# Optimization experiments

Measured on AMD Instinct MI355X. Metric: run time of the kernel, lower is better.

The kernel has to match this reference:

```python
import jax, jax.numpy as jnp
import numpy as np

B, S, D, H = 4, 2048, 1024, 16
d = D // H
SCALE = d ** -0.5


def setup_inputs() -> dict:
    key = jax.random.key(0)
    k1, k2, k3 = jax.random.split(key, 3)
    x = jax.random.normal(k1, (B, S, D), dtype=jnp.float32)
    # causal keep-mask (True = keep), shape (B, 1, S, S)
    causal = jnp.tril(jnp.ones((S, S), dtype=bool))
    mask = jnp.broadcast_to(causal[None, None, :, :], (B, 1, S, S))
    # nn.Linear(D, 3D, bias=False): weight (3D, D); out_proj weight (D, D)
    w_qkv = jax.random.normal(k2, (3 * D, D), dtype=jnp.float32) * (D ** -0.5)
    w_out = jax.random.normal(k3, (D, D), dtype=jnp.float32) * (D ** -0.5)
    return {"x": x, "mask": mask, "w_qkv": w_qkv, "w_out": w_out}


def reference(x, mask, w_qkv, w_out):
    # qkv projection: y = x @ W^T, split into q, k, v
    qkv = jnp.einsum('bsd,ed->bse', x, w_qkv)  # (B, S, 3D)
    q, k, v = jnp.split(qkv, 3, axis=-1)
    # (B, S, H, d) -> (B, H, S, d)
    q = q.reshape(B, S, H, d).transpose(0, 2, 1, 3)
    k = k.reshape(B, S, H, d).transpose(0, 2, 1, 3)
    v = v.reshape(B, S, H, d).transpose(0, 2, 1, 3)
    # scores (B, H, S, S)
    attn = jnp.einsum('bhqd,bhkd->bhqk', q, k) * SCALE
    attn = jnp.where(mask, attn, -jnp.inf)
    attn = jax.nn.softmax(attn, axis=-1)
    out = jnp.einsum('bhqk,bhkd->bhqd', attn, v)
    out = out.transpose(0, 2, 1, 3).reshape(B, S, D)
    out = jnp.einsum('bsd,ed->bse', out, w_out)
    return out, (k, v)
```

## Files before the change

kernel.cpp:

```cpp
#include <hip/hip_runtime.h>
#include <hip/hip_bf16.h>

typedef __bf16 bf16_t;
typedef bf16_t bf16x8 __attribute__((ext_vector_type(8)));
typedef bf16_t bf16x4 __attribute__((ext_vector_type(4)));
typedef float  f32x4  __attribute__((ext_vector_type(4)));
typedef float  f32x8  __attribute__((ext_vector_type(8)));
typedef float  f32x16 __attribute__((ext_vector_type(16)));

#define B_  4
#define S_  2048
#define D_  1024
#define H_  16
#define HD  64

#define QSCALE 0.1803368801111204f

#define KV_TILE_ELEMS 4096
#define KV_BH_ELEMS   262144

__device__ __forceinline__ void async_copy16(const void* g, void* l) {
    __builtin_amdgcn_global_load_lds((const __attribute__((address_space(1))) void*)g,
                                     (__attribute__((address_space(3))) void*)l,
                                     16, 0, 0);
}

__device__ __forceinline__ float fast_exp2(float x) {
    float r;
    asm("v_exp_f32 %0, %1" : "=v"(r) : "v"(x));
    return r;
}

template<int N>
__device__ __forceinline__ void wait_vmcnt() {
    if constexpr (N == 12)      asm volatile("s_waitcnt vmcnt(12)" ::: "memory");
    else if constexpr (N == 10) asm volatile("s_waitcnt vmcnt(10)" ::: "memory");
    else if constexpr (N == 8)  asm volatile("s_waitcnt vmcnt(8)"  ::: "memory");
    else if constexpr (N == 6)  asm volatile("s_waitcnt vmcnt(6)"  ::: "memory");
    else if constexpr (N == 5)  asm volatile("s_waitcnt vmcnt(5)"  ::: "memory");
    else if constexpr (N == 4)  asm volatile("s_waitcnt vmcnt(4)"  ::: "memory");
    else if constexpr (N == 3)  asm volatile("s_waitcnt vmcnt(3)"  ::: "memory");
    else                        asm volatile("s_waitcnt vmcnt(0)"  ::: "memory");
}

__global__ __launch_bounds__(256) void cvt_kernel(const float* __restrict__ in,
                                                  bf16_t* __restrict__ out, int n4) {
    int i = blockIdx.x * 256 + threadIdx.x;
    if (i >= n4) return;
    float4 f = ((const float4*)in)[i];
    bf16x4 o = { (bf16_t)f.x, (bf16_t)f.y, (bf16_t)f.z, (bf16_t)f.w };
    ((bf16x4*)out)[i] = o;
}

template<int WNS, int MREP, int NREP>
__device__ __forceinline__ void gemm_core256(const bf16_t* __restrict__ A,
                                             const bf16_t* __restrict__ Bt,
                                             int lda, int ldb, int m0, int n0, int K,
                                             bf16_t* LDS, f32x4 acc[MREP][NREP]) {
    constexpr int BM   = (8 / WNS) * MREP * 16;
    constexpr int BN   = WNS * NREP * 16;
    constexpr int BUFE = (BM + BN) * 32;
    constexpr int AI   = BM / 128;
    constexpr int BI   = BN / 128;
    constexpr int LPS  = AI + BI;

    const int lane = threadIdx.x & 63;
    const int wv   = threadIdx.x >> 6;
    const int wm   = wv / WNS, wn = wv % WNS;
    const int lo   = lane & 15, hi = lane >> 4;
    const int srd  = (lo >> 1) & 3;
    const int r_in = lane >> 2;
    const int csw  = (((lane & 3) ^ ((lane >> 3) & 3))) * 8;

    auto stage = [&](int t, int db) {
        const int k0 = t * 32;
        bf16_t* dstA = LDS + db * BUFE;
        bf16_t* dstB = dstA + BM * 32;
        #pragma unroll
        for (int i = 0; i < AI; ++i) {
            const int base = wv * (BM / 8) + i * 16;
            async_copy16(A + (size_t)(m0 + base + r_in) * lda + k0 + csw, dstA + base * 32);
        }
        #pragma unroll
        for (int i = 0; i < BI; ++i) {
            const int base = wv * (BN / 8) + i * 16;
            async_copy16(Bt + (size_t)(n0 + base + r_in) * ldb + k0 + csw, dstB + base * 32);
        }
    };

    auto compute = [&](int db) {
        const bf16_t* as = LDS + db * BUFE;
        const bf16_t* bs = as + BM * 32;
        const int kos = (hi ^ srd) * 8;
        bf16x8 bF[NREP];
        #pragma unroll
        for (int n = 0; n < NREP; ++n)
            bF[n] = *(const bf16x8*)(bs + (wn * (NREP * 16) + n * 16 + lo) * 32 + kos);
        #pragma unroll
        for (int m = 0; m < MREP; ++m) {
            bf16x8 aF = *(const bf16x8*)(as + (wm * (MREP * 16) + m * 16 + lo) * 32 + kos);
            #pragma unroll
            for (int n = 0; n < NREP; ++n)
                acc[m][n] = __builtin_amdgcn_mfma_f32_16x16x32_bf16(aF, bF[n], acc[m][n], 0, 0, 0);
        }
    };

    const int nt = K / 32;
    stage(0, 0); stage(1, 1); stage(2, 2);

    for (int t = 0; t < nt; ++t) {
        const int db = t % 3;
        if (t + 2 < nt)      wait_vmcnt<2 * LPS>();
        else if (t + 1 < nt) wait_vmcnt<LPS>();
        else                 wait_vmcnt<0>();
        __builtin_amdgcn_s_barrier();
        __builtin_amdgcn_sched_barrier(0);
        compute(db);
        __builtin_amdgcn_sched_barrier(0);
        __builtin_amdgcn_s_barrier();
        __builtin_amdgcn_sched_barrier(0);
        if (t + 3 < nt) stage(t + 3, db);
    }
}

__global__ __launch_bounds__(512) void gemm_qkv_kernel(const bf16_t* __restrict__ A,
                                                       const bf16_t* __restrict__ Bt,
                                                       float* __restrict__ out,
                                                       bf16_t* __restrict__ q_ws,
                                                       bf16_t* __restrict__ kv_frag) {
    __shared__ __align__(16) bf16_t LDS[3 * (256 + 384) * 32];
    const int m0 = (blockIdx.x >> 3) * 256;
    const int n0 = (blockIdx.x & 7) * 384;
    f32x4 acc[8][6];
    #pragma unroll
    for (int m = 0; m < 8; ++m)
        #pragma unroll
        for (int n = 0; n < 6; ++n) acc[m][n] = f32x4{0.f, 0.f, 0.f, 0.f};

    gemm_core256<4, 8, 6>(A, Bt, D_, D_, m0, n0, D_, LDS, acc);

    const int lane = threadIdx.x & 63, wv = threadIdx.x >> 6;
    const int wm = wv >> 2, wn = wv & 3;
    const int lo = lane & 15, hi = lane >> 4;
    #pragma unroll
    for (int m = 0; m < 8; ++m) {
        #pragma unroll
        for (int n = 0; n < 6; ++n) {
            const int gcol = n0 + wn * 96 + n * 16 + lo;
            const int sec  = gcol >> 10;
            const int e    = gcol & 1023;
            const int h    = e >> 6, dv = e & 63;
            #pragma unroll
            for (int j4 = 0; j4 < 4; ++j4) {
                const int grow = m0 + wm * 128 + m * 16 + hi * 4 + j4;
                const float v  = acc[m][n][j4];
                const int b = grow >> 11, s = grow & 2047;
                const size_t idx2 = ((((size_t)b * H_ + h) * S_ + s) << 6) + dv;
                if (sec == 0) {
                    q_ws[idx2] = (bf16_t)(v * QSCALE);
                } else if (sec == 1) {
                    out[8388608u + idx2] = v;
                    const int bh   = b * H_ + h;
                    const int tile = s >> 5, ql = s & 31;
                    const int c    = dv >> 4, hb = (dv >> 3) & 1, jj = dv & 7;
                    kv_frag[(((size_t)bh * 64 + tile) * 8 + c) * 512 + hb * 256 + ql * 8 + jj] = (bf16_t)v;
                } else {
                    out[16777216u + idx2] = v;
                }
            }
        }
    }
}

__global__ __launch_bounds__(256) void build_vfrag_kernel(const float* __restrict__ v_f32,
                                                          bf16_t* __restrict__ kv_frag) {
    __shared__ __align__(16) bf16_t T[64][72];
    const int bh = blockIdx.x;
    const int s0 = blockIdx.y * 64;
    const int t  = threadIdx.x;
    {
        const int sl  = t >> 2;
        const int dv0 = (t & 3) * 16;
        const float* src = v_f32 + ((size_t)bh * S_ + s0 + sl) * HD + dv0;
        float tmp[16];
        #pragma unroll
        for (int i = 0; i < 4; ++i) *(float4*)(tmp + i * 4) = ((const float4*)src)[i];
        #pragma unroll
        for (int i = 0; i < 16; ++i) T[dv0 + i][sl] = (bf16_t)tmp[i];
    }
    __syncthreads();
    {
        const int st = t >> 7;
        const int r  = t & 127;
        const int cc = r >> 5;
        const int l  = r & 31;
        const int khi = cc >> 1, hd = cc & 1;
        const int d   = hd * 32 + l;
        const int tile = (s0 >> 5) + st;
        bf16_t* dst = kv_frag + (((size_t)bh * 64 + tile) * 8 + 4 + cc) * 512 + l * 8;
        const int slb = st * 32 + khi * 16;
        *(bf16x8*)(dst)       = *(const bf16x8*)&T[d][slb];
        *(bf16x8*)(dst + 256) = *(const bf16x8*)&T[d][slb + 8];
    }
}

__global__ __launch_bounds__(256) void attn_kernel(const bf16_t* __restrict__ q_ws,
                                                   const bf16_t* __restrict__ kv_frag,
                                                   bf16_t* __restrict__ attn_ws) {
    __shared__ __align__(16) float MRG[2][2][64][20];
    __shared__ float LSUM[2][64];
    __shared__ __align__(16) bf16_t T[2][32][72];
    const int lane = threadIdx.x & 63;
    const int wv   = threadIdx.x >> 6;
    const int blk   = blockIdx.x;
    const int x     = blk & 7;
    const int r     = blk >> 3;
    const int bh    = x + 8 * (r & 7);
    const int pr    = wv >> 1;
    const int khalf = wv & 1;
    const int p     = (r >> 3) * 2 + pr;

    const int ql = lane & 31;
    const int hb = lane >> 5;
    const size_t kv_base = (size_t)bh * (S_ * HD);
    const int b = bh >> 4, h = bh & 15;

    const bf16_t* kvb = kv_frag + (size_t)bh * KV_BH_ELEMS + (size_t)lane * 8;

    auto load_k = [&](int tile, bf16x8 kf[4]) {
        const bf16_t* tp = kvb + (size_t)tile * KV_TILE_ELEMS;
        #pragma unroll
        for (int c = 0; c < 4; ++c) kf[c] = *(const bf16x8*)(tp + c * 512);
    };
    auto load_v = [&](int tile, bf16x8 vf[4]) {
        const bf16_t* tp = kvb + (size_t)tile * KV_TILE_ELEMS + 2048;
        #pragma unroll
        for (int i = 0; i < 4; ++i) vf[i] = *(const bf16x8*)(tp + i * 512);
    };

    #pragma unroll 1
    for (int pass = 0; pass < 2; ++pass) {
        const int qblock = pass ? (63 - p) : p;
        const int q0 = qblock * 32;
        const int nt  = qblock + 1;
        const int mid = nt >> 1;
        const int tstart = khalf ? mid : 0;
        const int tend   = khalf ? nt  : mid;

        bf16x8 qF[4];
        const bf16_t* qrow = q_ws + kv_base + (size_t)(q0 + ql) * HD + hb * 8;
        #pragma unroll
        for (int c = 0; c < 4; ++c) qF[c] = *(const bf16x8*)(qrow + 16 * c);

        f32x16 accT0 = {}, accT1 = {};
        float lsum = 0.f;

        auto compute_tile = [&](const bf16x8 kf[4], const bf16x8 vf[4], bool diag) {
            f32x16 s = {};
            #pragma unroll
            for (int c = 0; c < 4; ++c)
                s = __builtin_amdgcn_mfma_f32_32x32x16_bf16(kf[c], qF[c], s, 0, 0, 0);
            if (diag) {
                #pragma unroll
                for (int rr = 0; rr < 16; ++rr) {
                    const int kloc = (rr & 3) + 8 * (rr >> 2) + 4 * hb;
                    if (kloc > ql) s[rr] = -1e30f;
                }
            }
            #pragma unroll
            for (int rr = 0; rr < 16; ++rr) s[rr] = fast_exp2(s[rr]);
            f32x8 t8 = __builtin_shufflevector(s, s, 0, 1, 2, 3, 4, 5, 6, 7) +
                       __builtin_shufflevector(s, s, 8, 9, 10, 11, 12, 13, 14, 15);
            f32x4 t4 = __builtin_shufflevector(t8, t8, 0, 1, 2, 3) +
                       __builtin_shufflevector(t8, t8, 4, 5, 6, 7);
            lsum += (t4[0] + t4[1]) + (t4[2] + t4[3]);

            unsigned w[8];
            #pragma unroll
            for (int i = 0; i < 8; ++i) {
                unsigned d;
                asm("v_cvt_pk_bf16_f32 %0, %1, %2" : "=v"(d) : "v"(s[2 * i]), "v"(s[2 * i + 1]));
                w[i] = d;
            }
            union { unsigned u[4]; bf16x8 v; } pf0, pf1;
            {
                auto r0 = __builtin_amdgcn_permlane32_swap(w[0], w[2], false, false);
                auto r1 = __builtin_amdgcn_permlane32_swap(w[1], w[3], false, false);
                pf0.u[0] = r0[0]; pf0.u[1] = r1[0]; pf0.u[2] = r0[1]; pf0.u[3] = r1[1];
            }
            {
                auto r0 = __builtin_amdgcn_permlane32_swap(w[4], w[6], false, false);
                auto r1 = __builtin_amdgcn_permlane32_swap(w[5], w[7], false, false);
                pf1.u[0] = r0[0]; pf1.u[1] = r1[0]; pf1.u[2] = r0[1]; pf1.u[3] = r1[1];
            }

            accT0 = __builtin_amdgcn_mfma_f32_32x32x16_bf16(vf[0], pf0.v, accT0, 0, 0, 0);
            accT1 = __builtin_amdgcn_mfma_f32_32x32x16_bf16(vf[1], pf0.v, accT1, 0, 0, 0);
            accT0 = __builtin_amdgcn_mfma_f32_32x32x16_bf16(vf[2], pf1.v, accT0, 0, 0, 0);
            accT1 = __builtin_amdgcn_mfma_f32_32x32x16_bf16(vf[3], pf1.v, accT1, 0, 0, 0);
        };

        int t = tstart;
        for (; t + 1 < tend; t += 2) {
            bf16x8 kA[4], vA[4], kB[4], vB[4];
            load_k(t, kA);
            load_v(t, vA);
            load_k(t + 1, kB);
            load_v(t + 1, vB);
            compute_tile(kA, vA, t == qblock);
            compute_tile(kB, vB, (t + 1) == qblock);
        }
        if (t < tend) {
            bf16x8 kA[4], vA[4];
            load_k(t, kA);
            load_v(t, vA);
            compute_tile(kA, vA, t == qblock);
        }

        if (khalf) {
            *(f32x16*)&MRG[pr][0][lane][0] = accT0;
            *(f32x16*)&MRG[pr][1][lane][0] = accT1;
            LSUM[pr][lane] = lsum;
        }
        __syncthreads();
        if (!khalf) {
            accT0 += *(const f32x16*)&MRG[pr][0][lane][0];
            accT1 += *(const f32x16*)&MRG[pr][1][lane][0];
            lsum  += LSUM[pr][lane];
            const float ltot = lsum + __shfl_xor(lsum, 32, 64);
            const float inv  = 1.0f / ltot;
            #pragma unroll
            for (int rr = 0; rr < 16; ++rr) {
                const int dl = (rr & 3) + 8 * (rr >> 2) + 4 * hb;
                T[pr][ql][dl]      = (bf16_t)(accT0[rr] * inv);
                T[pr][ql][32 + dl] = (bf16_t)(accT1[rr] * inv);
            }
            asm volatile("s_waitcnt lgkmcnt(0)" ::: "memory");
            #pragma unroll
            for (int it = 0; it < 4; ++it) {
                const int ch  = it * 64 + lane;
                const int row = ch >> 3, c8 = ch & 7;
                bf16x8 o = *(const bf16x8*)&T[pr][row][c8 * 8];
                *(bf16x8*)(attn_ws + ((size_t)(b * S_ + q0 + row)) * D_ + h * HD + c8 * 8) = o;
            }
        }
        __syncthreads();
    }
}

__global__ __launch_bounds__(512) void gemm_out_kernel(const bf16_t* __restrict__ A,
                                                       const bf16_t* __restrict__ Bt,
                                                       float* __restrict__ out) {
    __shared__ __align__(16) bf16_t LDS[3 * (256 + 128) * 32];
    const int m0 = blockIdx.y * 256, n0 = blockIdx.x * 128;
    f32x4 acc[4][4];
    #pragma unroll
    for (int m = 0; m < 4; ++m)
        #pragma unroll
        for (int n = 0; n < 4; ++n) acc[m][n] = f32x4{0.f, 0.f, 0.f, 0.f};

    gemm_core256<2, 4, 4>(A, Bt, D_, D_, m0, n0, D_, LDS, acc);

    const int lane = threadIdx.x & 63, wv = threadIdx.x >> 6;
    const int wm = wv >> 1, wn = wv & 1;
    const int lo = lane & 15, hi = lane >> 4;
    #pragma unroll
    for (int m = 0; m < 4; ++m) {
        #pragma unroll
        for (int n = 0; n < 4; ++n) {
            const int gcol = n0 + wn * 64 + n * 16 + lo;
            #pragma unroll
            for (int j = 0; j < 4; ++j) {
                const int grow = m0 + wm * 64 + m * 16 + hi * 4 + j;
                out[(size_t)grow * D_ + gcol] = acc[m][n][j];
            }
        }
    }
}

extern "C" void kernel_launch(void* const* d_in, const int* in_sizes, int n_in,
                              void* d_out, int out_size, void* d_ws, size_t ws_size,
                              hipStream_t stream) {
    (void)in_sizes; (void)n_in; (void)out_size; (void)ws_size;
    const float* x     = (const float*)d_in[0];
    const float* w_qkv = (const float*)d_in[2];
    const float* w_out = (const float*)d_in[3];
    float* out = (float*)d_out;
    char* ws = (char*)d_ws;

    bf16_t* x_bf    = (bf16_t*)(ws);
    bf16_t* wqkv_bf = (bf16_t*)(ws + 16777216);
    bf16_t* wout_bf = (bf16_t*)(ws + 23068672);
    bf16_t* q_ws    = (bf16_t*)(ws + 25165824);
    bf16_t* kv_frag = (bf16_t*)(ws + 41943040);
    bf16_t* attn_ws = (bf16_t*)(ws + 75497472);

    cvt_kernel<<<8192, 256, 0, stream>>>(x, x_bf, 2097152);
    cvt_kernel<<<3072, 256, 0, stream>>>(w_qkv, wqkv_bf, 786432);
    cvt_kernel<<<1024, 256, 0, stream>>>(w_out, wout_bf, 262144);

    gemm_qkv_kernel<<<256, 512, 0, stream>>>(x_bf, wqkv_bf, out, q_ws, kv_frag);
    build_vfrag_kernel<<<dim3(64, 32), 256, 0, stream>>>(out + 16777216, kv_frag);
    attn_kernel<<<1024, 256, 0, stream>>>(q_ws, kv_frag, attn_ws);
    gemm_out_kernel<<<dim3(8, 32), 512, 0, stream>>>(attn_ws, wout_bf, out);
}
```

Measured before the change: 175.0 us.

## Rewrite QKV GEMM with 256x256 tiles and interleaved 8-wave async-load pipeline

Replaces the generic gemm_core256 call in the QKV projection with a hand-scheduled main loop. It uses 256x256 output tiles (384 blocks instead of 256), a 64-wide K step with double-buffered XOR-swizzled LDS, and async global-to-LDS loads split into halves that are issued between MFMA quarter-steps. The aim is better CU coverage on the 256-CU part and hiding load latency behind MFMA work using setprio and fine-grained barriers. In exchange it adds many more barriers per K step and needs a larger LDS footprint (128KB).

After: 176.5 us. About the same (+0.9%).

```diff
diff --git a/kernel.cpp b/kernel.cpp
--- a/kernel.cpp
+++ b/kernel.cpp
@@ -33,13 +33,11 @@
 
 template<int N>
 __device__ __forceinline__ void wait_vmcnt() {
-    if constexpr (N == 12)      asm volatile("s_waitcnt vmcnt(12)" ::: "memory");
-    else if constexpr (N == 10) asm volatile("s_waitcnt vmcnt(10)" ::: "memory");
+    if constexpr (N == 10)      asm volatile("s_waitcnt vmcnt(10)" ::: "memory");
     else if constexpr (N == 8)  asm volatile("s_waitcnt vmcnt(8)"  ::: "memory");
     else if constexpr (N == 6)  asm volatile("s_waitcnt vmcnt(6)"  ::: "memory");
     else if constexpr (N == 5)  asm volatile("s_waitcnt vmcnt(5)"  ::: "memory");
     else if constexpr (N == 4)  asm volatile("s_waitcnt vmcnt(4)"  ::: "memory");
-    else if constexpr (N == 3)  asm volatile("s_waitcnt vmcnt(3)"  ::: "memory");
     else                        asm volatile("s_waitcnt vmcnt(0)"  ::: "memory");
 }
 
@@ -128,25 +126,138 @@
                                                        float* __restrict__ out,
                                                        bf16_t* __restrict__ q_ws,
                                                        bf16_t* __restrict__ kv_frag) {
-    __shared__ __align__(16) bf16_t LDS[3 * (256 + 384) * 32];
-    const int m0 = (blockIdx.x >> 3) * 256;
-    const int n0 = (blockIdx.x & 7) * 384;
-    f32x4 acc[8][6];
+    __shared__ __align__(16) bf16_t LDS[65536];
+    constexpr int BOFF = 32768;
+    const int m0 = (blockIdx.x & 31) * 256;
+    const int n0 = (blockIdx.x >> 5) * 256;
+    const int tid  = (int)threadIdx.x;
+    const int lane = tid & 63;
+    const int wv   = tid >> 6;
+    const int wm   = wv >> 2, wn = wv & 3;
+    const int lo   = lane & 15, hi = lane >> 4;
+
+    f32x4 acc[8][4];
     #pragma unroll
     for (int m = 0; m < 8; ++m)
         #pragma unroll
-        for (int n = 0; n < 6; ++n) acc[m][n] = f32x4{0.f, 0.f, 0.f, 0.f};
-
-    gemm_core256<4, 8, 6>(A, Bt, D_, D_, m0, n0, D_, LDS, acc);
-
-    const int lane = threadIdx.x & 63, wv = threadIdx.x >> 6;
-    const int wm = wv >> 2, wn = wv & 3;
-    const int lo = lane & 15, hi = lane >> 4;
+        for (int n = 0; n < 4; ++n) acc[m][n] = f32x4{0.f, 0.f, 0.f, 0.f};
+
+    auto stage_half = [&](int T, int isB, int h) {
+        const int db = T & 1;
+        bf16_t* dst = LDS + (isB ? BOFF : 0) + (db * 2 + h) * 8192;
+        const bf16_t* src = isB ? Bt : A;
+        const int g0 = (isB ? n0 : m0) + h * 128;
+        const int k0 = T * 64;
+        #pragma unroll
+        for (int i = 0; i < 2; ++i) {
+            const int idx = i * 512 + tid;
+            const int row = idx >> 3, slot = idx & 7;
+            async_copy16(src + (size_t)(g0 + row) * 1024 + k0 + ((slot ^ (row & 7)) * 8),
+                         dst + i * 4096 + wv * 512);
+        }
+    };
+
+    stage_half(0, 0, 0); stage_half(0, 0, 1); stage_half(0, 1, 0); stage_half(0, 1, 1);
+    stage_half(1, 0, 0); stage_half(1, 0, 1); stage_half(1, 1, 0); stage_half(1, 1, 1);
+    wait_vmcnt<8>();
+    __builtin_amdgcn_s_barrier();
+    __builtin_amdgcn_sched_barrier(0);
+
+    #pragma unroll 1
+    for (int i = 0; i < 8; ++i) {
+        const bool s22 = (2 * i + 2 < 16);
+        const bool s23 = (2 * i + 3 < 16);
+        bf16x8 bF[4][2];
+
+        #pragma unroll
+        for (int q = 0; q < 4; ++q) {
+            bf16x8 aF[2][2];
+            #pragma unroll
+            for (int ml = 0; ml < 2; ++ml)
+                #pragma unroll
+                for (int kk = 0; kk < 2; ++kk) {
+                    const int row = (2 * q + ml) * 16 + lo;
+                    aF[ml][kk] = *(const bf16x8*)(LDS + wm * 8192 + row * 64 +
+                                                  (((kk * 4 + hi) ^ (lo & 7)) * 8));
+                }
+            if (q == 0) {
+                #pragma unroll
+                for (int n = 0; n < 4; ++n)
+                    #pragma unroll
+                    for (int kk = 0; kk < 2; ++kk) {
+                        const int row = (wn & 1) * 64 + n * 16 + lo;
+                        bF[n][kk] = *(const bf16x8*)(LDS + BOFF + (wn >> 1) * 8192 + row * 64 +
+                                                     (((kk * 4 + hi) ^ (lo & 7)) * 8));
+                    }
+                if (i >= 1) { stage_half(2 * i + 1, 0, 0); stage_half(2 * i + 1, 0, 1); }
+            } else if (q == 1) { if (s22) stage_half(2 * i + 2, 1, 0); }
+            else if (q == 2)   { if (s22) stage_half(2 * i + 2, 1, 1); }
+            __builtin_amdgcn_s_barrier();
+            asm volatile("s_waitcnt lgkmcnt(0)" ::: "memory");
+            __builtin_amdgcn_sched_barrier(0);
+            __builtin_amdgcn_s_setprio(1);
+            #pragma unroll
+            for (int kk = 0; kk < 2; ++kk)
+                #pragma unroll
+                for (int ml = 0; ml < 2; ++ml)
+                    #pragma unroll
+                    for (int n = 0; n < 4; ++n)
+                        acc[2 * q + ml][n] = __builtin_amdgcn_mfma_f32_16x16x32_bf16(
+                            aF[ml][kk], bF[n][kk], acc[2 * q + ml][n], 0, 0, 0);
+            __builtin_amdgcn_s_setprio(0);
+            if (q == 3) { if (s22) wait_vmcnt<4>(); else wait_vmcnt<0>(); }
+            __builtin_amdgcn_s_barrier();
+            __builtin_amdgcn_sched_barrier(0);
+        }
+
+        #pragma unroll
+        for (int q = 0; q < 4; ++q) {
+            bf16x8 aF[2][2];
+            #pragma unroll
+            for (int ml = 0; ml < 2; ++ml)
+                #pragma unroll
+                for (int kk = 0; kk < 2; ++kk) {
+                    const int row = (2 * q + ml) * 16 + lo;
+                    aF[ml][kk] = *(const bf16x8*)(LDS + (2 + wm) * 8192 + row * 64 +
+                                                  (((kk * 4 + hi) ^ (lo & 7)) * 8));
+                }
+            if (q == 0) {
+                #pragma unroll
+                for (int n = 0; n < 4; ++n)
+                    #pragma unroll
+                    for (int kk = 0; kk < 2; ++kk) {
+                        const int row = (wn & 1) * 64 + n * 16 + lo;
+                        bF[n][kk] = *(const bf16x8*)(LDS + BOFF + (2 + (wn >> 1)) * 8192 + row * 64 +
+                                                     (((kk * 4 + hi) ^ (lo & 7)) * 8));
+                    }
+                if (s22) stage_half(2 * i + 2, 0, 0);
+            } else if (q == 1) { if (s22) stage_half(2 * i + 2, 0, 1); }
+            else if (q == 2)   { if (s23) stage_half(2 * i + 3, 1, 0); }
+            else               { if (s23) stage_half(2 * i + 3, 1, 1); }
+            __builtin_amdgcn_s_barrier();
+            asm volatile("s_waitcnt lgkmcnt(0)" ::: "memory");
+            __builtin_amdgcn_sched_barrier(0);
+            __builtin_amdgcn_s_setprio(1);
+            #pragma unroll
+            for (int kk = 0; kk < 2; ++kk)
+                #pragma unroll
+                for (int ml = 0; ml < 2; ++ml)
+                    #pragma unroll
+                    for (int n = 0; n < 4; ++n)
+                        acc[2 * q + ml][n] = __builtin_amdgcn_mfma_f32_16x16x32_bf16(
+                            aF[ml][kk], bF[n][kk], acc[2 * q + ml][n], 0, 0, 0);
+            __builtin_amdgcn_s_setprio(0);
+            if (q == 3) { if (s23) wait_vmcnt<4>(); else wait_vmcnt<0>(); }
+            __builtin_amdgcn_s_barrier();
+            __builtin_amdgcn_sched_barrier(0);
+        }
+    }
+
     #pragma unroll
     for (int m = 0; m < 8; ++m) {
         #pragma unroll
-        for (int n = 0; n < 6; ++n) {
-            const int gcol = n0 + wn * 96 + n * 16 + lo;
+        for (int n = 0; n < 4; ++n) {
+            const int gcol = n0 + wn * 64 + n * 16 + lo;
             const int sec  = gcol >> 10;
             const int e    = gcol & 1023;
             const int h    = e >> 6, dv = e & 63;
@@ -399,7 +510,7 @@
     cvt_kernel<<<3072, 256, 0, stream>>>(w_qkv, wqkv_bf, 786432);
     cvt_kernel<<<1024, 256, 0, stream>>>(w_out, wout_bf, 262144);
 
-    gemm_qkv_kernel<<<256, 512, 0, stream>>>(x_bf, wqkv_bf, out, q_ws, kv_frag);
+    gemm_qkv_kernel<<<384, 512, 0, stream>>>(x_bf, wqkv_bf, out, q_ws, kv_frag);
     build_vfrag_kernel<<<dim3(64, 32), 256, 0, stream>>>(out + 16777216, kv_frag);
     attn_kernel<<<1024, 256, 0, stream>>>(q_ws, kv_frag, attn_ws);
     gemm_out_kernel<<<dim3(8, 32), 512, 0, stream>>>(attn_ws, wout_bf, out);
```
